# Performance work log

Hardware: AMD Instinct MI355X
Metric: run time of the kernel (lower is better)

## Reference

```python
import jax, jax.numpy as jnp
import numpy as np

CAPACITY_FACTOR = 1.0


def setup_inputs() -> dict:
    key = jax.random.key(0)
    ks = jax.random.split(key, 6)
    B, S, D, H, E = 4, 2048, 1024, 4096, 8
    scale_in = 1.0 / np.sqrt(D)
    scale_h = 1.0 / np.sqrt(H)
    return {
        "inputs": jax.random.normal(ks[0], (B, S, D), dtype=jnp.float32),
        "router_w": jax.random.normal(ks[1], (E, D), dtype=jnp.float32) * scale_in,
        "w1": jax.random.normal(ks[2], (E, D, H), dtype=jnp.float32) * scale_in,
        "b1": jnp.zeros((E, H), dtype=jnp.float32),
        "w2": jax.random.normal(ks[3], (E, H, D), dtype=jnp.float32) * scale_h,
        "b2": jnp.zeros((E, D), dtype=jnp.float32),
    }


def reference(inputs, router_w, w1, b1, w2, b2):
    B, S, D = inputs.shape
    E = router_w.shape[0]
    x = inputs.reshape(-1, D)                     # [T, D], T = B*S
    T = x.shape[0]
    top_k = int(CAPACITY_FACTOR * T / E)          # static: 1024

    # Router + softmax over experts (softmax_topk order), fp32 like the original
    router_logits = x @ router_w.T                # [T, E]
    all_probs = jax.nn.softmax(router_logits.astype(jnp.float32), axis=-1)

    # Expert-choice: each expert picks its top_k tokens
    weights, selected_tokens = jax.lax.top_k(all_probs.T, top_k)  # [E, K]

    # Gather tokens per expert: [E, K, D]
    xg = x[selected_tokens]

    # Per-expert MLP as grouped GEMMs (Linear -> GELU(exact) -> Linear)
    h = jax.nn.gelu(jnp.einsum("ekd,edh->ekh", xg, w1) + b1[:, None, :],
                    approximate=False)
    out = jnp.einsum("ekh,ehd->ekd", h, w2) + b2[:, None, :]   # [E, K, D]

    # Weighted scatter-add combine (indices unique within an expert;
    # cross-expert duplicates accumulate, matching the per-expert += loop)
    out = out * weights[..., None].astype(out.dtype)
    results = jnp.zeros_like(x).at[selected_tokens.reshape(-1)].add(
        out.reshape(-1, D))

    return results.reshape(B, S, D), router_logits, selected_tokens
```

## Files before the change

kernel.cpp:

```cpp
#include <hip/hip_runtime.h>
#include <hip/hip_bf16.h>
#include <math.h>

#define T_TOK 8192
#define E_EXP 8
#define D_DIM 1024
#define H_DIM 4096
#define K_CAP 1024

typedef __attribute__((ext_vector_type(8))) short short8;
typedef __attribute__((ext_vector_type(4))) float floatx4;

typedef __attribute__((address_space(3))) unsigned int lds_u32_t;
typedef __attribute__((address_space(1))) unsigned int gbl_u32_t;
#define ASYNC_CP16(gptr, lptr) \
  __builtin_amdgcn_global_load_lds((gbl_u32_t*)(gptr), (lds_u32_t*)(lptr), 16, 0, 0)

static __device__ __forceinline__ unsigned int f2bf_u(float f) {
  union { float f; unsigned int u; } v; v.f = f;
  unsigned int r = v.u + 0x7FFF + ((v.u >> 16) & 1);
  return r >> 16;
}

__global__ __launch_bounds__(256) void zero_kernel(float* __restrict__ p, int n4) {
  int i = blockIdx.x * 256 + threadIdx.x;
  if (i < n4) ((floatx4*)p)[i] = (floatx4)0.0f;
}

__global__ __launch_bounds__(256)
void convert_kernel(const float* __restrict__ x, unsigned short* __restrict__ xb, int n4) {
  int i = blockIdx.x * 256 + threadIdx.x;
  if (i < n4) {
    float4 v = ((const float4*)x)[i];
    uint2 u;
    u.x = f2bf_u(v.x) | (f2bf_u(v.y) << 16);
    u.y = f2bf_u(v.z) | (f2bf_u(v.w) << 16);
    ((uint2*)xb)[i] = u;
  }
}

template <int KD, int ND>
__global__ __launch_bounds__(256)
void transpose_kernel(const float* __restrict__ w, unsigned short* __restrict__ wt) {
  int e = blockIdx.z;
  int n0 = blockIdx.x * 64, k0 = blockIdx.y * 64;
  __shared__ float ts[64][65];
  int tid = threadIdx.x;
  int rr = tid >> 4;
  int cc = (tid & 15) * 4;
  const float* src = w + ((size_t)e * KD + k0 + rr) * ND + n0 + cc;
#pragma unroll
  for (int it = 0; it < 4; it++) {
    float4 v = *(const float4*)(src + (size_t)it * 16 * ND);
    int r = rr + it * 16;
    ts[r][cc + 0] = v.x; ts[r][cc + 1] = v.y; ts[r][cc + 2] = v.z; ts[r][cc + 3] = v.w;
  }
  __syncthreads();
  int n = tid >> 3;
  int k8 = (tid & 7) * 8;
#pragma unroll
  for (int it = 0; it < 2; it++) {
    int nn = n + it * 32;
    unsigned int u[4];
#pragma unroll
    for (int j = 0; j < 4; j++)
      u[j] = f2bf_u(ts[k8 + 2 * j][nn]) | (f2bf_u(ts[k8 + 2 * j + 1][nn]) << 16);
    *(uint4*)&wt[((size_t)e * ND + n0 + nn) * KD + k0 + k8] = *(uint4*)u;
  }
}

__global__ __launch_bounds__(256)
void router_kernel(const float* __restrict__ x, const float* __restrict__ rw,
                   float* __restrict__ logits_out, float* __restrict__ probs_ws,
                   unsigned long long* __restrict__ keys_ws) {
  int t = blockIdx.x;
  int tid = threadIdx.x;
  int lane = tid & 63, wid = tid >> 6;
  __shared__ float xs[D_DIM];
  __shared__ double dred[4 * E_EXP];
  __shared__ double dlog[E_EXP];
  for (int i = tid; i < D_DIM; i += 256) xs[i] = x[(size_t)t * D_DIM + i];
  __syncthreads();
#pragma unroll
  for (int e = 0; e < E_EXP; e++) {
    double s = 0.0;
#pragma unroll
    for (int i = 0; i < 4; i++) {
      int d = tid + i * 256;
      s += (double)xs[d] * (double)rw[e * D_DIM + d];
    }
#pragma unroll
    for (int off = 32; off > 0; off >>= 1) s += __shfl_down(s, off, 64);
    if (lane == 0) dred[wid * E_EXP + e] = s;
  }
  __syncthreads();
  if (tid < E_EXP) {
    double s = dred[tid] + dred[E_EXP + tid] + dred[2 * E_EXP + tid] + dred[3 * E_EXP + tid];
    dlog[tid] = s;
    logits_out[(size_t)t * E_EXP + tid] = (float)s;
  }
  __syncthreads();
  if (tid == 0) {
    double m = dlog[0];
#pragma unroll
    for (int e = 1; e < E_EXP; e++) m = dlog[e] > m ? dlog[e] : m;
    double ex[E_EXP], Z = 0.0;
#pragma unroll
    for (int e = 0; e < E_EXP; e++) { ex[e] = exp(dlog[e] - m); Z += ex[e]; }
#pragma unroll
    for (int e = 0; e < E_EXP; e++) {
      double p = ex[e] / Z;
      probs_ws[e * T_TOK + t] = (float)p;
      unsigned long long b = (unsigned long long)__double_as_longlong(p);
      keys_ws[e * T_TOK + t] = (b & ~8191ULL) | (unsigned long long)(8191 - t);
    }
  }
}

__global__ __launch_bounds__(256)
void topk_kernel(const unsigned long long* __restrict__ keys_ws,
                 const float* __restrict__ probs_ws,
                 int* __restrict__ sel_ws, float* __restrict__ wt_ws,
                 float* __restrict__ selout) {
  int e = blockIdx.x >> 5, seg = blockIdx.x & 31;
  int tid = threadIdx.x;
  const unsigned long long* keys = keys_ws + (size_t)e * T_TOK;
  __shared__ unsigned long long kbuf[2048];
  int t = seg * 256 + tid;
  unsigned long long own = keys[t];
  int rank = 0;
  for (int pass = 0; pass < 4; pass++) {
    __syncthreads();
    for (int j = tid; j < 2048; j += 256) kbuf[j] = keys[pass * 2048 + j];
    __syncthreads();
#pragma unroll 8
    for (int j = 0; j < 2048; j++) rank += (kbuf[j] > own);
  }
  if (rank < K_CAP) {
    sel_ws[e * K_CAP + rank] = t;
    wt_ws[e * K_CAP + rank] = probs_ws[e * T_TOK + t];
    selout[e * K_CAP + rank] = (float)t;
  }
}

template <int MODE, int KDIM, int NDIM, int SPLIT, int NT>
__global__ __launch_bounds__(256)
void gemm_kernel(const unsigned short* __restrict__ abase,
                 const unsigned short* __restrict__ bt,
                 const float* __restrict__ bias,
                 const int* __restrict__ sel,
                 const float* __restrict__ wt,
                 unsigned short* __restrict__ hout,
                 float* __restrict__ results) {
  int e = blockIdx.x;
  int rest = blockIdx.y;
  int s = rest & (SPLIT - 1);
  int nt = (rest / SPLIT) % NT;
  int mt = rest / (SPLIT * NT);
  int n0 = nt * 128;
  int m0 = mt * 128;
  const int KCH = KDIM / SPLIT;
  int kbase = s * KCH;

  int tid = threadIdx.x;
  int lane = tid & 63, wid = tid >> 6;
  int wave_m = wid >> 1, wave_n = wid & 1;
  __shared__ unsigned short As[128 * 32];
  __shared__ unsigned short Bs[128 * 32];

  int r0 = tid >> 2;
  int coff = (tid & 3) * 8;
  const unsigned short* aptr0;
  const unsigned short* aptr1;
  if (MODE == 1) {
    aptr0 = abase + (size_t)sel[e * K_CAP + m0 + r0] * KDIM + kbase + coff;
    aptr1 = abase + (size_t)sel[e * K_CAP + m0 + 64 + r0] * KDIM + kbase + coff;
  } else {
    aptr0 = abase + ((size_t)e * K_CAP + m0 + r0) * KDIM + kbase + coff;
    aptr1 = aptr0 + (size_t)64 * KDIM;
  }
  const unsigned short* bptr0 = bt + ((size_t)e * NDIM + n0 + r0) * KDIM + kbase + coff;
  const unsigned short* bptr1 = bptr0 + (size_t)64 * KDIM;

  char* ldsA0 = (char*)As + wid * 1024;
  char* ldsA1 = ldsA0 + 4096;
  char* ldsB0 = (char*)Bs + wid * 1024;
  char* ldsB1 = ldsB0 + 4096;

  floatx4 acc[4][4];
#pragma unroll
  for (int i = 0; i < 4; i++)
#pragma unroll
    for (int j = 0; j < 4; j++) acc[i][j] = (floatx4)0.0f;

  int lm = lane & 15;
  int q8 = (lane >> 4) * 8;

  for (int k0 = 0; k0 < KCH; k0 += 32) {
    ASYNC_CP16(aptr0, ldsA0);
    ASYNC_CP16(aptr1, ldsA1);
    ASYNC_CP16(bptr0, ldsB0);
    ASYNC_CP16(bptr1, ldsB1);
    aptr0 += 32; aptr1 += 32; bptr0 += 32; bptr1 += 32;
    __syncthreads();
    short8 av[4], bv[4];
#pragma unroll
    for (int i = 0; i < 4; i++) {
      av[i] = *(const short8*)&As[(wave_m * 64 + i * 16 + lm) * 32 + q8];
      bv[i] = *(const short8*)&Bs[(wave_n * 64 + i * 16 + lm) * 32 + q8];
    }
#pragma unroll
    for (int mi = 0; mi < 4; mi++)
#pragma unroll
      for (int ni = 0; ni < 4; ni++)
        acc[mi][ni] = __builtin_amdgcn_mfma_f32_16x16x32_bf16(av[mi], bv[ni], acc[mi][ni], 0, 0, 0);
    __syncthreads();
  }

  int quad = lane >> 4;
  float bs[4];
#pragma unroll
  for (int ni = 0; ni < 4; ni++)
    bs[ni] = (MODE == 1 || s == 0) ? bias[e * NDIM + n0 + wave_n * 64 + ni * 16 + lm] : 0.0f;
#pragma unroll
  for (int mi = 0; mi < 4; mi++) {
#pragma unroll
    for (int rg = 0; rg < 4; rg++) {
      int m_l = wave_m * 64 + mi * 16 + quad * 4 + rg;
      int m_g = m0 + m_l;
      if (MODE == 1) {
#pragma unroll
        for (int ni = 0; ni < 4; ni++) {
          int n_l = wave_n * 64 + ni * 16 + lm;
          float v = acc[mi][ni][rg] + bs[ni];
          float gl = 0.5f * v * (1.0f + erff(v * 0.70710678118f));
          hout[((size_t)e * K_CAP + m_g) * H_DIM + n0 + n_l] = (unsigned short)f2bf_u(gl);
        }
      } else {
        int tok = sel[e * K_CAP + m_g];
        float wgt = wt[e * K_CAP + m_g];
#pragma unroll
        for (int ni = 0; ni < 4; ni++) {
          int n_l = wave_n * 64 + ni * 16 + lm;
          float v = (acc[mi][ni][rg] + bs[ni]) * wgt;
          atomicAdd(&results[(size_t)tok * D_DIM + n0 + n_l], v);
        }
      }
    }
  }
}

extern "C" void kernel_launch(void* const* d_in, const int* in_sizes, int n_in,
                              void* d_out, int out_size, void* d_ws, size_t ws_size,
                              hipStream_t stream) {
  const float* x  = (const float*)d_in[0];
  const float* rw = (const float*)d_in[1];
  const float* w1 = (const float*)d_in[2];
  const float* b1 = (const float*)d_in[3];
  const float* w2 = (const float*)d_in[4];
  const float* b2 = (const float*)d_in[5];

  float* out_res = (float*)d_out;
  float* out_log = out_res + (size_t)T_TOK * D_DIM;
  float* out_sel = out_log + (size_t)T_TOK * E_EXP;

  char* ws = (char*)d_ws;
  float* probs_ws = (float*)ws;
  unsigned long long* keys_ws = (unsigned long long*)(ws + 262144);
  int* sel_ws = (int*)(ws + 786432);
  float* wt_ws = (float*)(ws + 819200);
  unsigned short* x_bf = (unsigned short*)(ws + 1048576);
  unsigned short* h_ws = (unsigned short*)(ws + 17825792);
  unsigned short* t_buf = (unsigned short*)(ws + 84934656);

  zero_kernel<<<(T_TOK * D_DIM / 4 + 255) / 256, 256, 0, stream>>>(out_res, T_TOK * D_DIM / 4);

  convert_kernel<<<(T_TOK * D_DIM / 4 + 255) / 256, 256, 0, stream>>>(
      x, x_bf, T_TOK * D_DIM / 4);

  router_kernel<<<T_TOK, 256, 0, stream>>>(x, rw, out_log, probs_ws, keys_ws);

  topk_kernel<<<256, 256, 0, stream>>>(keys_ws, probs_ws, sel_ws, wt_ws, out_sel);

  transpose_kernel<D_DIM, H_DIM><<<dim3(H_DIM / 64, D_DIM / 64, E_EXP), 256, 0, stream>>>(
      w1, t_buf);

  gemm_kernel<1, D_DIM, H_DIM, 1, H_DIM / 128>
      <<<dim3(E_EXP, (H_DIM / 128) * (K_CAP / 128)), 256, 0, stream>>>(
      x_bf, t_buf, b1, sel_ws, wt_ws, h_ws, nullptr);

  transpose_kernel<H_DIM, D_DIM><<<dim3(D_DIM / 64, H_DIM / 64, E_EXP), 256, 0, stream>>>(
      w2, t_buf);

  gemm_kernel<2, H_DIM, D_DIM, 2, D_DIM / 128>
      <<<dim3(E_EXP, (D_DIM / 128) * (K_CAP / 128) * 2), 256, 0, stream>>>(
      h_ws, t_buf, b2, sel_ws, wt_ws, nullptr, out_res);
}
```

Measured before the change: 740.5 us.

## Switch GEMMs to 32x32x16 MFMA with 64-wide K tiles and fuse bf16 convert into router

Rewrites both expert GEMMs to use 32x32x16 bf16 MFMA instructions with a 2x2 tile per wave and a 64-wide K step, which halves the number of barrier pairs and changes the LDS read pattern. It also adds launch_bounds occupancy hints and reorders the grid for the first GEMM. The bf16 conversion of the input is folded into the router kernel, which already stages each token row in LDS, so one full pass over x is dropped. The trade-offs are larger LDS use per block and more accumulator registers per wave.

Result: faster. 685.2 us (-7.5%).

```diff
diff --git a/kernel.cpp b/kernel.cpp
--- a/kernel.cpp
+++ b/kernel.cpp
@@ -10,6 +10,7 @@
 
 typedef __attribute__((ext_vector_type(8))) short short8;
 typedef __attribute__((ext_vector_type(4))) float floatx4;
+typedef __attribute__((ext_vector_type(16))) float floatx16;
 
 typedef __attribute__((address_space(3))) unsigned int lds_u32_t;
 typedef __attribute__((address_space(1))) unsigned int gbl_u32_t;
@@ -25,18 +26,6 @@
 __global__ __launch_bounds__(256) void zero_kernel(float* __restrict__ p, int n4) {
   int i = blockIdx.x * 256 + threadIdx.x;
   if (i < n4) ((floatx4*)p)[i] = (floatx4)0.0f;
-}
-
-__global__ __launch_bounds__(256)
-void convert_kernel(const float* __restrict__ x, unsigned short* __restrict__ xb, int n4) {
-  int i = blockIdx.x * 256 + threadIdx.x;
-  if (i < n4) {
-    float4 v = ((const float4*)x)[i];
-    uint2 u;
-    u.x = f2bf_u(v.x) | (f2bf_u(v.y) << 16);
-    u.y = f2bf_u(v.z) | (f2bf_u(v.w) << 16);
-    ((uint2*)xb)[i] = u;
-  }
 }
 
 template <int KD, int ND>
@@ -72,7 +61,8 @@
 __global__ __launch_bounds__(256)
 void router_kernel(const float* __restrict__ x, const float* __restrict__ rw,
                    float* __restrict__ logits_out, float* __restrict__ probs_ws,
-                   unsigned long long* __restrict__ keys_ws) {
+                   unsigned long long* __restrict__ keys_ws,
+                   unsigned short* __restrict__ x_bf) {
   int t = blockIdx.x;
   int tid = threadIdx.x;
   int lane = tid & 63, wid = tid >> 6;
@@ -81,6 +71,13 @@
   __shared__ double dlog[E_EXP];
   for (int i = tid; i < D_DIM; i += 256) xs[i] = x[(size_t)t * D_DIM + i];
   __syncthreads();
+  {
+    int i4 = tid * 4;
+    uint2 u;
+    u.x = f2bf_u(xs[i4 + 0]) | (f2bf_u(xs[i4 + 1]) << 16);
+    u.y = f2bf_u(xs[i4 + 2]) | (f2bf_u(xs[i4 + 3]) << 16);
+    ((uint2*)(x_bf + (size_t)t * D_DIM))[tid] = u;
+  }
 #pragma unroll
   for (int e = 0; e < E_EXP; e++) {
     double s = 0.0;
@@ -143,111 +140,149 @@
   }
 }
 
-template <int MODE, int KDIM, int NDIM, int SPLIT, int NT>
-__global__ __launch_bounds__(256)
-void gemm_kernel(const unsigned short* __restrict__ abase,
-                 const unsigned short* __restrict__ bt,
-                 const float* __restrict__ bias,
-                 const int* __restrict__ sel,
-                 const float* __restrict__ wt,
-                 unsigned short* __restrict__ hout,
-                 float* __restrict__ results) {
-  int e = blockIdx.x;
-  int rest = blockIdx.y;
-  int s = rest & (SPLIT - 1);
-  int nt = (rest / SPLIT) % NT;
-  int mt = rest / (SPLIT * NT);
-  int n0 = nt * 128;
-  int m0 = mt * 128;
-  const int KCH = KDIM / SPLIT;
-  int kbase = s * KCH;
-
+template <int MODE, int KDIM, int NDIM>
+__device__ __forceinline__ void gemm_core(
+    int e, int m0, int n0, int kbase, int kch, bool add_bias,
+    const unsigned short* __restrict__ abase,
+    const unsigned short* __restrict__ bt,
+    const float* __restrict__ bias,
+    const int* __restrict__ sel,
+    const float* __restrict__ wt,
+    unsigned short* __restrict__ hout,
+    float* __restrict__ results) {
+  __shared__ unsigned short As[128 * 64];
+  __shared__ unsigned short Bs[128 * 64];
   int tid = threadIdx.x;
-  int lane = tid & 63, wid = tid >> 6;
-  int wave_m = wid >> 1, wave_n = wid & 1;
-  __shared__ unsigned short As[128 * 32];
-  __shared__ unsigned short Bs[128 * 32];
-
-  int r0 = tid >> 2;
-  int coff = (tid & 3) * 8;
-  const unsigned short* aptr0;
-  const unsigned short* aptr1;
+  int lane = tid & 63, w = tid >> 6;
+  int wave_m = w >> 1, wave_n = w & 1;
+
+  int srow = lane >> 2;
+  int scol = (lane & 3) * 8;
+  int rowA0 = w * 16 + srow;
+  int rowA1 = (4 + w) * 16 + srow;
+  const unsigned short *arow0, *arow1;
   if (MODE == 1) {
-    aptr0 = abase + (size_t)sel[e * K_CAP + m0 + r0] * KDIM + kbase + coff;
-    aptr1 = abase + (size_t)sel[e * K_CAP + m0 + 64 + r0] * KDIM + kbase + coff;
+    arow0 = abase + (size_t)sel[e * K_CAP + m0 + rowA0] * KDIM + kbase + scol;
+    arow1 = abase + (size_t)sel[e * K_CAP + m0 + rowA1] * KDIM + kbase + scol;
   } else {
-    aptr0 = abase + ((size_t)e * K_CAP + m0 + r0) * KDIM + kbase + coff;
-    aptr1 = aptr0 + (size_t)64 * KDIM;
-  }
-  const unsigned short* bptr0 = bt + ((size_t)e * NDIM + n0 + r0) * KDIM + kbase + coff;
-  const unsigned short* bptr1 = bptr0 + (size_t)64 * KDIM;
-
-  char* ldsA0 = (char*)As + wid * 1024;
-  char* ldsA1 = ldsA0 + 4096;
-  char* ldsB0 = (char*)Bs + wid * 1024;
-  char* ldsB1 = ldsB0 + 4096;
-
-  floatx4 acc[4][4];
-#pragma unroll
-  for (int i = 0; i < 4; i++)
-#pragma unroll
-    for (int j = 0; j < 4; j++) acc[i][j] = (floatx4)0.0f;
-
-  int lm = lane & 15;
-  int q8 = (lane >> 4) * 8;
-
-  for (int k0 = 0; k0 < KCH; k0 += 32) {
-    ASYNC_CP16(aptr0, ldsA0);
-    ASYNC_CP16(aptr1, ldsA1);
-    ASYNC_CP16(bptr0, ldsB0);
-    ASYNC_CP16(bptr1, ldsB1);
-    aptr0 += 32; aptr1 += 32; bptr0 += 32; bptr1 += 32;
+    arow0 = abase + ((size_t)e * K_CAP + m0 + rowA0) * KDIM + kbase + scol;
+    arow1 = abase + ((size_t)e * K_CAP + m0 + rowA1) * KDIM + kbase + scol;
+  }
+  const unsigned short* brow0 = bt + ((size_t)e * NDIM + n0 + rowA0) * KDIM + kbase + scol;
+  const unsigned short* brow1 = bt + ((size_t)e * NDIM + n0 + rowA1) * KDIM + kbase + scol;
+
+  char* lA0 = (char*)As + w * 1024;
+  char* lA1 = (char*)As + (4 + w) * 1024;
+  char* lA2 = (char*)As + (8 + w) * 1024;
+  char* lA3 = (char*)As + (12 + w) * 1024;
+  char* lB0 = (char*)Bs + w * 1024;
+  char* lB1 = (char*)Bs + (4 + w) * 1024;
+  char* lB2 = (char*)Bs + (8 + w) * 1024;
+  char* lB3 = (char*)Bs + (12 + w) * 1024;
+
+  floatx16 acc[2][2];
+#pragma unroll
+  for (int i = 0; i < 2; i++)
+#pragma unroll
+    for (int j = 0; j < 2; j++) acc[i][j] = (floatx16)0.0f;
+
+  int am = lane & 31;
+  int k8 = (lane >> 5) * 8;
+
+  for (int k0 = 0; k0 < kch; k0 += 64) {
+    ASYNC_CP16(arow0, lA0);
+    ASYNC_CP16(arow1, lA1);
+    ASYNC_CP16(arow0 + 32, lA2);
+    ASYNC_CP16(arow1 + 32, lA3);
+    ASYNC_CP16(brow0, lB0);
+    ASYNC_CP16(brow1, lB1);
+    ASYNC_CP16(brow0 + 32, lB2);
+    ASYNC_CP16(brow1 + 32, lB3);
+    arow0 += 64; arow1 += 64; brow0 += 64; brow1 += 64;
     __syncthreads();
-    short8 av[4], bv[4];
-#pragma unroll
-    for (int i = 0; i < 4; i++) {
-      av[i] = *(const short8*)&As[(wave_m * 64 + i * 16 + lm) * 32 + q8];
-      bv[i] = *(const short8*)&Bs[(wave_n * 64 + i * 16 + lm) * 32 + q8];
-    }
-#pragma unroll
-    for (int mi = 0; mi < 4; mi++)
-#pragma unroll
-      for (int ni = 0; ni < 4; ni++)
-        acc[mi][ni] = __builtin_amdgcn_mfma_f32_16x16x32_bf16(av[mi], bv[ni], acc[mi][ni], 0, 0, 0);
+    short8 av[2][4], bv[2][4];
+#pragma unroll
+    for (int t = 0; t < 2; t++)
+#pragma unroll
+      for (int kk = 0; kk < 4; kk++) {
+        int idx = (kk >> 1) * 4096 + (kk & 1) * 16 + k8;
+        av[t][kk] = *(const short8*)&As[idx + (wave_m * 64 + t * 32 + am) * 32];
+        bv[t][kk] = *(const short8*)&Bs[idx + (wave_n * 64 + t * 32 + am) * 32];
+      }
+#pragma unroll
+    for (int kk = 0; kk < 4; kk++)
+#pragma unroll
+      for (int ti = 0; ti < 2; ti++)
+#pragma unroll
+        for (int tj = 0; tj < 2; tj++)
+          acc[ti][tj] = __builtin_amdgcn_mfma_f32_32x32x16_bf16(
+              av[ti][kk], bv[tj][kk], acc[ti][tj], 0, 0, 0);
     __syncthreads();
   }
 
-  int quad = lane >> 4;
-  float bs[4];
-#pragma unroll
-  for (int ni = 0; ni < 4; ni++)
-    bs[ni] = (MODE == 1 || s == 0) ? bias[e * NDIM + n0 + wave_n * 64 + ni * 16 + lm] : 0.0f;
-#pragma unroll
-  for (int mi = 0; mi < 4; mi++) {
-#pragma unroll
-    for (int rg = 0; rg < 4; rg++) {
-      int m_l = wave_m * 64 + mi * 16 + quad * 4 + rg;
-      int m_g = m0 + m_l;
-      if (MODE == 1) {
-#pragma unroll
-        for (int ni = 0; ni < 4; ni++) {
-          int n_l = wave_n * 64 + ni * 16 + lm;
-          float v = acc[mi][ni][rg] + bs[ni];
+  int hi = lane >> 5;
+#pragma unroll
+  for (int ti = 0; ti < 2; ti++) {
+    int rbase = wave_m * 64 + ti * 32 + hi * 4;
+    if (MODE == 1) {
+#pragma unroll
+      for (int tj = 0; tj < 2; tj++) {
+        int col = n0 + wave_n * 64 + tj * 32 + am;
+        float bv_ = bias[e * NDIM + col];
+#pragma unroll
+        for (int r = 0; r < 16; r++) {
+          int m_l = rbase + (r & 3) + 8 * (r >> 2);
+          float v = acc[ti][tj][r] + bv_;
           float gl = 0.5f * v * (1.0f + erff(v * 0.70710678118f));
-          hout[((size_t)e * K_CAP + m_g) * H_DIM + n0 + n_l] = (unsigned short)f2bf_u(gl);
+          hout[((size_t)e * K_CAP + m0 + m_l) * H_DIM + col] = (unsigned short)f2bf_u(gl);
         }
-      } else {
-        int tok = sel[e * K_CAP + m_g];
-        float wgt = wt[e * K_CAP + m_g];
-#pragma unroll
-        for (int ni = 0; ni < 4; ni++) {
-          int n_l = wave_n * 64 + ni * 16 + lm;
-          float v = (acc[mi][ni][rg] + bs[ni]) * wgt;
-          atomicAdd(&results[(size_t)tok * D_DIM + n0 + n_l], v);
+      }
+    } else {
+      int toks[16]; float wgts[16];
+#pragma unroll
+      for (int r = 0; r < 16; r++) {
+        int m_l = rbase + (r & 3) + 8 * (r >> 2);
+        toks[r] = sel[e * K_CAP + m0 + m_l];
+        wgts[r] = wt[e * K_CAP + m0 + m_l];
+      }
+#pragma unroll
+      for (int tj = 0; tj < 2; tj++) {
+        int col = n0 + wave_n * 64 + tj * 32 + am;
+        float bv_ = add_bias ? bias[e * NDIM + col] : 0.0f;
+#pragma unroll
+        for (int r = 0; r < 16; r++) {
+          float v = (acc[ti][tj][r] + bv_) * wgts[r];
+          atomicAdd(&results[(size_t)toks[r] * D_DIM + col], v);
         }
       }
     }
   }
+}
+
+__global__ __launch_bounds__(256, 2)
+void moe_gemm1(const unsigned short* __restrict__ x_bf,
+               const unsigned short* __restrict__ w1t,
+               const float* __restrict__ b1,
+               const int* __restrict__ sel,
+               unsigned short* __restrict__ h) {
+  gemm_core<1, D_DIM, H_DIM>(blockIdx.z, blockIdx.y * 128, blockIdx.x * 128,
+                             0, D_DIM, true, x_bf, w1t, b1, sel, nullptr, h, nullptr);
+}
+
+__global__ __launch_bounds__(256, 2)
+void moe_gemm2(const unsigned short* __restrict__ h,
+               const unsigned short* __restrict__ w2t,
+               const float* __restrict__ b2,
+               const int* __restrict__ sel,
+               const float* __restrict__ wt,
+               float* __restrict__ results) {
+  int e = blockIdx.x;
+  int rest = blockIdx.y;
+  int s = rest & 1;
+  int nt = (rest >> 1) & 7;
+  int mt = rest >> 4;
+  gemm_core<2, H_DIM, D_DIM>(e, mt * 128, nt * 128, s * (H_DIM / 2), H_DIM / 2,
+                             s == 0, h, w2t, b2, sel, wt, nullptr, results);
 }
 
 extern "C" void kernel_launch(void* const* d_in, const int* in_sizes, int n_in,
@@ -275,24 +310,19 @@
 
   zero_kernel<<<(T_TOK * D_DIM / 4 + 255) / 256, 256, 0, stream>>>(out_res, T_TOK * D_DIM / 4);
 
-  convert_kernel<<<(T_TOK * D_DIM / 4 + 255) / 256, 256, 0, stream>>>(
-      x, x_bf, T_TOK * D_DIM / 4);
-
-  router_kernel<<<T_TOK, 256, 0, stream>>>(x, rw, out_log, probs_ws, keys_ws);
+  router_kernel<<<T_TOK, 256, 0, stream>>>(x, rw, out_log, probs_ws, keys_ws, x_bf);
 
   topk_kernel<<<256, 256, 0, stream>>>(keys_ws, probs_ws, sel_ws, wt_ws, out_sel);
 
   transpose_kernel<D_DIM, H_DIM><<<dim3(H_DIM / 64, D_DIM / 64, E_EXP), 256, 0, stream>>>(
       w1, t_buf);
 
-  gemm_kernel<1, D_DIM, H_DIM, 1, H_DIM / 128>
-      <<<dim3(E_EXP, (H_DIM / 128) * (K_CAP / 128)), 256, 0, stream>>>(
-      x_bf, t_buf, b1, sel_ws, wt_ws, h_ws, nullptr);
+  moe_gemm1<<<dim3(H_DIM / 128, K_CAP / 128, E_EXP), 256, 0, stream>>>(
+      x_bf, t_buf, b1, sel_ws, h_ws);
 
   transpose_kernel<H_DIM, D_DIM><<<dim3(D_DIM / 64, H_DIM / 64, E_EXP), 256, 0, stream>>>(
       w2, t_buf);
 
-  gemm_kernel<2, H_DIM, D_DIM, 2, D_DIM / 128>
-      <<<dim3(E_EXP, (D_DIM / 128) * (K_CAP / 128) * 2), 256, 0, stream>>>(
-      h_ws, t_buf, b2, sel_ws, wt_ws, nullptr, out_res);
-}
+  moe_gemm2<<<dim3(E_EXP, (D_DIM / 128) * (K_CAP / 128) * 2), 256, 0, stream>>>(
+      h_ws, t_buf, b2, sel_ws, wt_ws, out_res);
+}
```
